# Optimization experiments

Measured on AMD Instinct MI355X. Metric: run time of the kernel, lower is better.

## Reference

```python
import jax, jax.numpy as jnp
import numpy as np

DN = ('NCHW', 'OIHW', 'NCHW')


def dwconv(x, w, b, pad, dil=(1, 1)):
    # depthwise conv: w is (C, 1, kh, kw), feature_group_count = C
    y = jax.lax.conv_general_dilated(
        x, w, window_strides=(1, 1), padding=[pad[0], pad[1]],
        rhs_dilation=dil, dimension_numbers=DN, feature_group_count=w.shape[0])
    return y + b[None, :, None, None]


def setup_inputs() -> dict:
    key = jax.random.key(0)
    ks = jax.random.split(key, 18)
    dim, B, H, W = 512, 8, 64, 64
    s = 0.1  # keep depthwise chain numerically tame
    inp = {'x': jax.random.normal(ks[0], (B, dim, H, W), jnp.float32)}
    shapes = {
        'w0': (dim, 1, 5, 5), 'w0_1': (dim, 1, 1, 7), 'w0_2': (dim, 1, 7, 1),
        'w1_1': (dim, 1, 1, 11), 'w1_2': (dim, 1, 11, 1),
        'w2_1': (dim, 1, 1, 21), 'w2_2': (dim, 1, 21, 1),
        'w3': (dim, dim, 1, 1),
    }
    i = 1
    for name, shp in shapes.items():
        fan_in = shp[1] * shp[2] * shp[3]
        inp[name] = jax.random.normal(ks[i], shp, jnp.float32) * (s / np.sqrt(fan_in))
        inp['b' + name[1:]] = jax.random.normal(ks[i + 1], (dim,), jnp.float32) * 0.01
        i += 2
    return inp


def reference(x, w0, b0, w0_1, b0_1, w0_2, b0_2, w1_1, b1_1, w1_2, b1_2,
              w2_1, b2_1, w2_2, b2_2, w3, b3):
    u = x
    attn = dwconv(x, w0, b0, ((2, 2), (2, 2)))                       # 5x5 dw
    a0 = dwconv(attn, w0_1, b0_1, ((0, 0), (9, 9)), (3, 3))          # 1x7 d3
    a0 = dwconv(a0, w0_2, b0_2, ((9, 9), (0, 0)), (3, 3))            # 7x1 d3
    a1 = dwconv(attn, w1_1, b1_1, ((0, 0), (15, 15)), (3, 3))        # 1x11 d3
    a1 = dwconv(a1, w1_2, b1_2, ((15, 15), (0, 0)), (3, 3))          # 11x1 d3
    a2 = dwconv(attn, w2_1, b2_1, ((0, 0), (30, 30)), (3, 3))        # 1x21 d3
    a2 = dwconv(a2, w2_2, b2_2, ((30, 30), (0, 0)), (3, 3))          # 21x1 d3
    attn = attn + a0 + a1 + a2
    # 1x1 pointwise conv (dense channel mix)
    attn = jax.lax.conv_general_dilated(
        attn, w3, (1, 1), [(0, 0), (0, 0)], dimension_numbers=DN)
    attn = attn + b3[None, :, None, None]
    return attn * u
```

## Files before the change

### kernel.cpp

```cpp
#include <hip/hip_runtime.h>
#include <hip/hip_bf16.h>
#include <stdint.h>

typedef __attribute__((ext_vector_type(4))) float f32x4;
typedef __attribute__((ext_vector_type(8))) short s16x8;

#define XS_STRIDE 68
#define AS_STRIDE 132
#define AS_OFF 32
#define HT_STRIDE 68

__device__ static inline void load_lds_16B(const void* g, void* l) {
    __builtin_amdgcn_global_load_lds((const __attribute__((address_space(1))) void*)g,
                                     (__attribute__((address_space(3))) void*)l,
                                     16, 0, 0);
}


template<int K, int P, int P4>
__device__ __forceinline__ void branch_h(const float* __restrict__ wh, float bh,
                                         int r, int cq,
                                         const float* as_, float* ht_) {
    constexpr int SH = P4 - P;
    constexpr int NW = 16 + 2 * P;
    constexpr int NV = (NW + SH + 3) / 4;
    float vb[NV * 4];
    const float* src = as_ + r * AS_STRIDE + (AS_OFF - P4) + cq;
#pragma unroll
    for (int i = 0; i < NV; ++i) {
        f32x4 tmp = *(const f32x4*)(src + 4 * i);
        vb[4 * i + 0] = tmp[0]; vb[4 * i + 1] = tmp[1];
        vb[4 * i + 2] = tmp[2]; vb[4 * i + 3] = tmp[3];
    }
    float wr[K];
#pragma unroll
    for (int i = 0; i < K; ++i) wr[i] = wh[i];
    float out[16];
#pragma unroll
    for (int j = 0; j < 16; ++j) {
        float a = bh;
#pragma unroll
        for (int i = 0; i < K; ++i) a += vb[SH + j + 3 * i] * wr[i];
        out[j] = a;
    }
#pragma unroll
    for (int i = 0; i < 4; ++i) {
        f32x4 o = {out[4 * i], out[4 * i + 1], out[4 * i + 2], out[4 * i + 3]};
        *(f32x4*)(ht_ + r * HT_STRIDE + cq + 4 * i) = o;
    }
}

template<int K, int P>
__device__ __forceinline__ void branch_v(const float* __restrict__ wv, float bv,
                                         int cc, int r0,
                                         const float* ht_, float* ss) {
    constexpr int NW = 16 + 2 * P;
    float u[NW];
#pragma unroll
    for (int k = 0; k < NW; ++k) {
        int rr = r0 - P + k;
        u[k] = (rr >= 0 && rr < 64) ? ht_[rr * HT_STRIDE + cc] : 0.0f;
    }
    float wr[K];
#pragma unroll
    for (int i = 0; i < K; ++i) wr[i] = wv[i];
#pragma unroll
    for (int j = 0; j < 16; ++j) {
        float a = bv;
#pragma unroll
        for (int i = 0; i < K; ++i) a += u[j + 3 * i] * wr[i];
        ss[j] += a;
    }
}

__global__ __launch_bounds__(256, 2)
void k1_dw(const float* __restrict__ x,
           const float* __restrict__ w0,   const float* __restrict__ b0,
           const float* __restrict__ w0_1, const float* __restrict__ b0_1,
           const float* __restrict__ w0_2, const float* __restrict__ b0_2,
           const float* __restrict__ w1_1, const float* __restrict__ b1_1,
           const float* __restrict__ w1_2, const float* __restrict__ b1_2,
           const float* __restrict__ w2_1, const float* __restrict__ b2_1,
           const float* __restrict__ w2_2, const float* __restrict__ b2_2,
           __hip_bfloat16* __restrict__ s_out) {
    __shared__ float xs[64 * XS_STRIDE];
    __shared__ float as[64 * AS_STRIDE];
    __shared__ float ht[64 * HT_STRIDE];

    const int t = threadIdx.x;
    const int bid = blockIdx.x;
    const int c = bid & 511;
    const size_t pbase = (size_t)bid * 4096;

    {
        f32x4 z = {0.f, 0.f, 0.f, 0.f};
        f32x4* asv = (f32x4*)as;
#pragma unroll
        for (int i = 0; i < 9; ++i) {
            int idx = t + i * 256;
            if (idx < 64 * AS_STRIDE / 4) asv[idx] = z;
        }
        if (t < 64) {
            xs[t * XS_STRIDE + 0] = 0.f; xs[t * XS_STRIDE + 1] = 0.f;
            xs[t * XS_STRIDE + 66] = 0.f; xs[t * XS_STRIDE + 67] = 0.f;
        }
    }
    {
        const int r = t >> 2, cq = (t & 3) * 16;
        const f32x4* gx = (const f32x4*)(x + pbase + r * 64 + cq);
        f32x4* dst = (f32x4*)(xs + r * XS_STRIDE + 2 + cq);
#pragma unroll
        for (int i = 0; i < 4; ++i) dst[i] = gx[i];
    }
    __syncthreads();

    {
        const int r = t >> 2, cq = (t & 3) * 16;
        const float bias = b0[c];
        float acc[16];
#pragma unroll
        for (int j = 0; j < 16; ++j) acc[j] = bias;
        const float* wc = w0 + c * 25;
#pragma unroll
        for (int dr = 0; dr < 5; ++dr) {
            int rr = r + dr - 2;
            if (rr >= 0 && rr <= 63) {
                float v[20];
                const float* src = xs + rr * XS_STRIDE + cq;
#pragma unroll
                for (int i = 0; i < 5; ++i) {
                    f32x4 tmp = *(const f32x4*)(src + 4 * i);
                    v[4 * i + 0] = tmp[0]; v[4 * i + 1] = tmp[1];
                    v[4 * i + 2] = tmp[2]; v[4 * i + 3] = tmp[3];
                }
                const float* wrow = wc + dr * 5;
#pragma unroll
                for (int j = 0; j < 16; ++j)
#pragma unroll
                    for (int dc = 0; dc < 5; ++dc)
                        acc[j] += v[j + dc] * wrow[dc];
            }
        }
#pragma unroll
        for (int i = 0; i < 4; ++i) {
            f32x4 o = {acc[4 * i], acc[4 * i + 1], acc[4 * i + 2], acc[4 * i + 3]};
            *(f32x4*)(as + r * AS_STRIDE + AS_OFF + cq + 4 * i) = o;
        }
    }
    __syncthreads();

    const int r = t >> 2, cq = (t & 3) * 16;
    const int cc = t & 63, r0 = (t >> 6) * 16;

    float ss[16];
#pragma unroll
    for (int j = 0; j < 16; ++j) ss[j] = as[(r0 + j) * AS_STRIDE + AS_OFF + cc];

    branch_h<7, 9, 12>(w0_1 + c * 7, b0_1[c], r, cq, as, ht);
    __syncthreads();
    branch_v<7, 9>(w0_2 + c * 7, b0_2[c], cc, r0, ht, ss);
    __syncthreads();
    branch_h<11, 15, 16>(w1_1 + c * 11, b1_1[c], r, cq, as, ht);
    __syncthreads();
    branch_v<11, 15>(w1_2 + c * 11, b1_2[c], cc, r0, ht, ss);
    __syncthreads();
    branch_h<21, 30, 32>(w2_1 + c * 21, b2_1[c], r, cq, as, ht);
    __syncthreads();
    branch_v<21, 30>(w2_2 + c * 21, b2_2[c], cc, r0, ht, ss);

#pragma unroll
    for (int j = 0; j < 16; ++j)
        s_out[pbase + (size_t)(r0 + j) * 64 + cc] = __float2bfloat16(ss[j]);
}

__global__ __launch_bounds__(256, 4)
void k2_transpose(const __hip_bfloat16* __restrict__ s_px,
                  __hip_bfloat16* __restrict__ st) {
    __shared__ short tile[64][66];
    const int b = blockIdx.x;
    const int n = b >> 9, rem = b & 511;
    const int cib = rem >> 6, pxb = rem & 63;
    const int t = threadIdx.x;

    {
        const int row = t >> 2, chunk = (t & 3) * 16;
        const __hip_bfloat16* src =
            s_px + ((size_t)(n * 512 + cib * 64 + row)) * 4096 + pxb * 64 + chunk;
        s16x8 v0 = *(const s16x8*)(src);
        s16x8 v1 = *(const s16x8*)(src + 8);
#pragma unroll
        for (int k = 0; k < 8; ++k) {
            tile[row][chunk + k] = v0[k];
            tile[row][chunk + 8 + k] = v1[k];
        }
    }
    __syncthreads();
    {
        const int pxl = t >> 2, cich = (t & 3) * 16;
        s16x8 o0, o1;
#pragma unroll
        for (int k = 0; k < 8; ++k) {
            o0[k] = tile[cich + k][pxl];
            o1[k] = tile[cich + 8 + k][pxl];
        }
        __hip_bfloat16* dst =
            st + ((size_t)(n * 4096 + pxb * 64 + pxl)) * 512 + cib * 64 + cich;
        *(s16x8*)dst = o0;
        *(s16x8*)(dst + 8) = o1;
    }
}

__global__ __launch_bounds__(256, 4)
void k2b_cast(const float* __restrict__ w3, __hip_bfloat16* __restrict__ w3b) {
    const int i = (blockIdx.x * 256 + threadIdx.x) * 4;
    f32x4 v = *(const f32x4*)(w3 + i);
    union { __hip_bfloat16 h[4]; uint32_t u[2]; } pk;
#pragma unroll
    for (int k = 0; k < 4; ++k) pk.h[k] = __float2bfloat16(v[k]);
    *(uint32_t*)((char*)(w3b + i)) = pk.u[0];
    *(uint32_t*)((char*)(w3b + i) + 4) = pk.u[1];
}

__global__ __launch_bounds__(256, 2)
void k3_gemm(const __hip_bfloat16* __restrict__ w3b,
             const __hip_bfloat16* __restrict__ st,
             const float* __restrict__ b3,
             const float* __restrict__ x,
             float* __restrict__ out) {
    __shared__ __hip_bfloat16 As[128 * 64];
    __shared__ __hip_bfloat16 Bs[128 * 64];

    const int t = threadIdx.x;
    const int lane = t & 63, wv = t >> 6;
    const int waveM = wv & 1, waveN = wv >> 1;
    const int coBase = blockIdx.x * 128;
    const int nb = blockIdx.y;
    const int n = nb >> 5, pxTile = nb & 31;
    const int pxBase = pxTile * 128;
    const int lr = lane & 15, lq = lane >> 4;

    f32x4 acc[4][4] = {};

    for (int k0 = 0; k0 < 512; k0 += 64) {
#pragma unroll
        for (int s = 0; s < 4; ++s) {
            const int seg = wv * 4 + s;
            const int rowg = seg * 8 + (lane >> 3);
            const int kcol = k0 + (lane & 7) * 8;
            const __hip_bfloat16* ga = w3b + (size_t)(coBase + rowg) * 512 + kcol;
            load_lds_16B(ga, &As[seg * 512]);
            const __hip_bfloat16* gb =
                st + ((size_t)(n * 4096 + pxBase + rowg)) * 512 + kcol;
            load_lds_16B(gb, &Bs[seg * 512]);
        }
        __syncthreads();
#pragma unroll
        for (int kk = 0; kk < 64; kk += 32) {
            s16x8 af[4], bf[4];
#pragma unroll
            for (int m = 0; m < 4; ++m)
                af[m] = *(const s16x8*)&As[(waveM * 64 + m * 16 + lr) * 64 + kk + lq * 8];
#pragma unroll
            for (int nn = 0; nn < 4; ++nn)
                bf[nn] = *(const s16x8*)&Bs[(waveN * 64 + nn * 16 + lr) * 64 + kk + lq * 8];
#pragma unroll
            for (int m = 0; m < 4; ++m)
#pragma unroll
                for (int nn = 0; nn < 4; ++nn)
                    acc[m][nn] = __builtin_amdgcn_mfma_f32_16x16x32_bf16(
                        af[m], bf[nn], acc[m][nn], 0, 0, 0);
        }
        __syncthreads();
    }

#pragma unroll
    for (int m = 0; m < 4; ++m) {
#pragma unroll
        for (int nn = 0; nn < 4; ++nn) {
            const int px = pxBase + waveN * 64 + nn * 16 + lr;
#pragma unroll
            for (int j = 0; j < 4; ++j) {
                const int co = coBase + waveM * 64 + m * 16 + lq * 4 + j;
                const size_t idx = ((size_t)(n * 512 + co)) * 4096 + px;
                out[idx] = (acc[m][nn][j] + b3[co]) * x[idx];
            }
        }
    }
}

extern "C" void kernel_launch(void* const* d_in, const int* in_sizes, int n_in,
                              void* d_out, int out_size, void* d_ws, size_t ws_size,
                              hipStream_t stream) {
    (void)in_sizes; (void)n_in; (void)out_size; (void)ws_size;
    const float* x    = (const float*)d_in[0];
    const float* w0   = (const float*)d_in[1];
    const float* b0   = (const float*)d_in[2];
    const float* w0_1 = (const float*)d_in[3];
    const float* b0_1 = (const float*)d_in[4];
    const float* w0_2 = (const float*)d_in[5];
    const float* b0_2 = (const float*)d_in[6];
    const float* w1_1 = (const float*)d_in[7];
    const float* b1_1 = (const float*)d_in[8];
    const float* w1_2 = (const float*)d_in[9];
    const float* b1_2 = (const float*)d_in[10];
    const float* w2_1 = (const float*)d_in[11];
    const float* b2_1 = (const float*)d_in[12];
    const float* w2_2 = (const float*)d_in[13];
    const float* b2_2 = (const float*)d_in[14];
    const float* w3   = (const float*)d_in[15];
    const float* b3   = (const float*)d_in[16];
    float* out = (float*)d_out;

    __hip_bfloat16* s_px = (__hip_bfloat16*)d_out;
    __hip_bfloat16* st   = (__hip_bfloat16*)d_ws;
    __hip_bfloat16* w3b  = (__hip_bfloat16*)((char*)d_ws + ((size_t)32 << 20));

    k1_dw<<<4096, 256, 0, stream>>>(x, w0, b0, w0_1, b0_1, w0_2, b0_2,
                                    w1_1, b1_1, w1_2, b1_2, w2_1, b2_1,
                                    w2_2, b2_2, s_px);
    k2_transpose<<<4096, 256, 0, stream>>>(s_px, st);
    k2b_cast<<<256, 256, 0, stream>>>(w3, w3b);
    k3_gemm<<<dim3(4, 256), 256, 0, stream>>>(w3b, st, b3, x, out);
}
```

Before: 274.7 us.

## Double k1 threads with 8-wide work, alias LDS buffers, swizzle GEMM block order

```diff
diff --git a/kernel.cpp b/kernel.cpp
--- a/kernel.cpp
+++ b/kernel.cpp
@@ -22,8 +22,8 @@
                                          int r, int cq,
                                          const float* as_, float* ht_) {
     constexpr int SH = P4 - P;
-    constexpr int NW = 16 + 2 * P;
-    constexpr int NV = (NW + SH + 3) / 4;
+    constexpr int NW = 8 + 2 * P;
+    constexpr int NV = (SH + NW + 3) / 4;
     float vb[NV * 4];
     const float* src = as_ + r * AS_STRIDE + (AS_OFF - P4) + cq;
 #pragma unroll
@@ -35,16 +35,16 @@
     float wr[K];
 #pragma unroll
     for (int i = 0; i < K; ++i) wr[i] = wh[i];
-    float out[16];
-#pragma unroll
-    for (int j = 0; j < 16; ++j) {
+    float out[8];
+#pragma unroll
+    for (int j = 0; j < 8; ++j) {
         float a = bh;
 #pragma unroll
         for (int i = 0; i < K; ++i) a += vb[SH + j + 3 * i] * wr[i];
         out[j] = a;
     }
 #pragma unroll
-    for (int i = 0; i < 4; ++i) {
+    for (int i = 0; i < 2; ++i) {
         f32x4 o = {out[4 * i], out[4 * i + 1], out[4 * i + 2], out[4 * i + 3]};
         *(f32x4*)(ht_ + r * HT_STRIDE + cq + 4 * i) = o;
     }
@@ -54,7 +54,7 @@
 __device__ __forceinline__ void branch_v(const float* __restrict__ wv, float bv,
                                          int cc, int r0,
                                          const float* ht_, float* ss) {
-    constexpr int NW = 16 + 2 * P;
+    constexpr int NW = 8 + 2 * P;
     float u[NW];
 #pragma unroll
     for (int k = 0; k < NW; ++k) {
@@ -65,7 +65,7 @@
 #pragma unroll
     for (int i = 0; i < K; ++i) wr[i] = wv[i];
 #pragma unroll
-    for (int j = 0; j < 16; ++j) {
+    for (int j = 0; j < 8; ++j) {
         float a = bv;
 #pragma unroll
         for (int i = 0; i < K; ++i) a += u[j + 3 * i] * wr[i];
@@ -73,7 +73,7 @@
     }
 }
 
-__global__ __launch_bounds__(256, 2)
+__global__ __launch_bounds__(512, 6)
 void k1_dw(const float* __restrict__ x,
            const float* __restrict__ w0,   const float* __restrict__ b0,
            const float* __restrict__ w0_1, const float* __restrict__ b0_1,
@@ -83,9 +83,8 @@
            const float* __restrict__ w2_1, const float* __restrict__ b2_1,
            const float* __restrict__ w2_2, const float* __restrict__ b2_2,
            __hip_bfloat16* __restrict__ s_out) {
-    __shared__ float xs[64 * XS_STRIDE];
     __shared__ float as[64 * AS_STRIDE];
-    __shared__ float ht[64 * HT_STRIDE];
+    __shared__ float xs_ht[64 * XS_STRIDE];
 
     const int t = threadIdx.x;
     const int bid = blockIdx.x;
@@ -96,80 +95,77 @@
         f32x4 z = {0.f, 0.f, 0.f, 0.f};
         f32x4* asv = (f32x4*)as;
 #pragma unroll
-        for (int i = 0; i < 9; ++i) {
-            int idx = t + i * 256;
+        for (int i = 0; i < 5; ++i) {
+            int idx = t + i * 512;
             if (idx < 64 * AS_STRIDE / 4) asv[idx] = z;
         }
         if (t < 64) {
-            xs[t * XS_STRIDE + 0] = 0.f; xs[t * XS_STRIDE + 1] = 0.f;
-            xs[t * XS_STRIDE + 66] = 0.f; xs[t * XS_STRIDE + 67] = 0.f;
-        }
-    }
-    {
-        const int r = t >> 2, cq = (t & 3) * 16;
+            xs_ht[t * XS_STRIDE + 0] = 0.f; xs_ht[t * XS_STRIDE + 1] = 0.f;
+            xs_ht[t * XS_STRIDE + 66] = 0.f; xs_ht[t * XS_STRIDE + 67] = 0.f;
+        }
+    }
+    const int r = t >> 3, cq = (t & 7) * 8;
+    {
         const f32x4* gx = (const f32x4*)(x + pbase + r * 64 + cq);
-        f32x4* dst = (f32x4*)(xs + r * XS_STRIDE + 2 + cq);
-#pragma unroll
-        for (int i = 0; i < 4; ++i) dst[i] = gx[i];
-    }
-    __syncthreads();
-
-    {
-        const int r = t >> 2, cq = (t & 3) * 16;
+        f32x4* dst = (f32x4*)(xs_ht + r * XS_STRIDE + 2 + cq);
+        dst[0] = gx[0]; dst[1] = gx[1];
+    }
+    __syncthreads();
+
+    {
         const float bias = b0[c];
-        float acc[16];
-#pragma unroll
-        for (int j = 0; j < 16; ++j) acc[j] = bias;
+        float acc[8];
+#pragma unroll
+        for (int j = 0; j < 8; ++j) acc[j] = bias;
         const float* wc = w0 + c * 25;
 #pragma unroll
         for (int dr = 0; dr < 5; ++dr) {
             int rr = r + dr - 2;
             if (rr >= 0 && rr <= 63) {
-                float v[20];
-                const float* src = xs + rr * XS_STRIDE + cq;
-#pragma unroll
-                for (int i = 0; i < 5; ++i) {
+                float v[12];
+                const float* src = xs_ht + rr * XS_STRIDE + cq;
+#pragma unroll
+                for (int i = 0; i < 3; ++i) {
                     f32x4 tmp = *(const f32x4*)(src + 4 * i);
                     v[4 * i + 0] = tmp[0]; v[4 * i + 1] = tmp[1];
                     v[4 * i + 2] = tmp[2]; v[4 * i + 3] = tmp[3];
                 }
                 const float* wrow = wc + dr * 5;
 #pragma unroll
-                for (int j = 0; j < 16; ++j)
+                for (int j = 0; j < 8; ++j)
 #pragma unroll
                     for (int dc = 0; dc < 5; ++dc)
                         acc[j] += v[j + dc] * wrow[dc];
             }
         }
 #pragma unroll
-        for (int i = 0; i < 4; ++i) {
+        for (int i = 0; i < 2; ++i) {
             f32x4 o = {acc[4 * i], acc[4 * i + 1], acc[4 * i + 2], acc[4 * i + 3]};
             *(f32x4*)(as + r * AS_STRIDE + AS_OFF + cq + 4 * i) = o;
         }
     }
     __syncthreads();
 
-    const int r = t >> 2, cq = (t & 3) * 16;
-    const int cc = t & 63, r0 = (t >> 6) * 16;
-
-    float ss[16];
-#pragma unroll
-    for (int j = 0; j < 16; ++j) ss[j] = as[(r0 + j) * AS_STRIDE + AS_OFF + cc];
-
-    branch_h<7, 9, 12>(w0_1 + c * 7, b0_1[c], r, cq, as, ht);
-    __syncthreads();
-    branch_v<7, 9>(w0_2 + c * 7, b0_2[c], cc, r0, ht, ss);
-    __syncthreads();
-    branch_h<11, 15, 16>(w1_1 + c * 11, b1_1[c], r, cq, as, ht);
-    __syncthreads();
-    branch_v<11, 15>(w1_2 + c * 11, b1_2[c], cc, r0, ht, ss);
-    __syncthreads();
-    branch_h<21, 30, 32>(w2_1 + c * 21, b2_1[c], r, cq, as, ht);
-    __syncthreads();
-    branch_v<21, 30>(w2_2 + c * 21, b2_2[c], cc, r0, ht, ss);
-
-#pragma unroll
-    for (int j = 0; j < 16; ++j)
+    const int cc = t & 63, r0 = (t >> 6) * 8;
+
+    float ss[8];
+#pragma unroll
+    for (int j = 0; j < 8; ++j) ss[j] = as[(r0 + j) * AS_STRIDE + AS_OFF + cc];
+
+    branch_h<7, 9, 12>(w0_1 + c * 7, b0_1[c], r, cq, as, xs_ht);
+    __syncthreads();
+    branch_v<7, 9>(w0_2 + c * 7, b0_2[c], cc, r0, xs_ht, ss);
+    __syncthreads();
+    branch_h<11, 15, 16>(w1_1 + c * 11, b1_1[c], r, cq, as, xs_ht);
+    __syncthreads();
+    branch_v<11, 15>(w1_2 + c * 11, b1_2[c], cc, r0, xs_ht, ss);
+    __syncthreads();
+    branch_h<21, 30, 32>(w2_1 + c * 21, b2_1[c], r, cq, as, xs_ht);
+    __syncthreads();
+    branch_v<21, 30>(w2_2 + c * 21, b2_2[c], cc, r0, xs_ht, ss);
+
+#pragma unroll
+    for (int j = 0; j < 8; ++j)
         s_out[pbase + (size_t)(r0 + j) * 64 + cc] = __float2bfloat16(ss[j]);
 }
 
@@ -233,8 +229,9 @@
     const int t = threadIdx.x;
     const int lane = t & 63, wv = t >> 6;
     const int waveM = wv & 1, waveN = wv >> 1;
-    const int coBase = blockIdx.x * 128;
-    const int nb = blockIdx.y;
+    const int d = blockIdx.x;
+    const int coBase = ((d >> 3) & 3) * 128;
+    const int nb = (d & 7) | ((d >> 5) << 3);
     const int n = nb >> 5, pxTile = nb & 31;
     const int pxBase = pxTile * 128;
     const int lr = lane & 15, lq = lane >> 4;
@@ -315,10 +312,10 @@
     __hip_bfloat16* st   = (__hip_bfloat16*)d_ws;
     __hip_bfloat16* w3b  = (__hip_bfloat16*)((char*)d_ws + ((size_t)32 << 20));
 
-    k1_dw<<<4096, 256, 0, stream>>>(x, w0, b0, w0_1, b0_1, w0_2, b0_2,
+    k1_dw<<<4096, 512, 0, stream>>>(x, w0, b0, w0_1, b0_1, w0_2, b0_2,
                                     w1_1, b1_1, w1_2, b1_2, w2_1, b2_1,
                                     w2_2, b2_2, s_px);
     k2_transpose<<<4096, 256, 0, stream>>>(s_px, st);
     k2b_cast<<<256, 256, 0, stream>>>(w3, w3b);
-    k3_gemm<<<dim3(4, 256), 256, 0, stream>>>(w3b, st, b3, x, out);
-}
+    k3_gemm<<<1024, 256, 0, stream>>>(w3b, st, b3, x, out);
+}
```

Result: slower. 427.9 us (+55.8%).
